# Performance work log

Measured on AMD Instinct MI355X. Metric: run time of the kernel, lower is better.

## Reference

```python
import jax, jax.numpy as jnp
import numpy as np

N, D, S = 8192, 512, 5000
L_MAX, G_MAX, C_MAX = 512, 16, 6
MARGIN = 0.0
EPS = 1e-12


def setup_inputs() -> dict:
    key = jax.random.key(0)
    k1, k2, k3, k4, k5, k6 = jax.random.split(key, 6)
    return {
        'embeddings': jax.random.normal(k1, (N, D), dtype=jnp.float32),
        'labels': jax.random.randint(k2, (N,), 0, L_MAX),
        'graph_ids': jax.random.randint(k3, (N,), 0, G_MAX),
        'categories': jax.random.randint(k4, (N,), 0, C_MAX),
        'idx1': jax.random.randint(k5, (S,), 0, N),
        'idx2': jax.random.randint(k6, (S,), 0, N),
    }


def reference(embeddings, labels, graph_ids, categories, idx1, idx2):
    # L2-normalize rows (F.normalize, p=2, dim=1, eps=1e-12)
    norms = jnp.maximum(jnp.linalg.norm(embeddings, axis=1, keepdims=True), EPS)
    e = embeddings / norms
    n = e.shape[0]

    conserved = categories < 3  # [n]
    r = jnp.arange(n)
    upper_tri = r[:, None] < r[None, :]                     # i < j
    same_label = labels[:, None] == labels[None, :]
    diff_graph = graph_ids[:, None] != graph_ids[None, :]
    valid_pos = (upper_tri & same_label & diff_graph
                 & conserved[:, None] & conserved[None, :])  # [n, n] bool

    sims = e @ e.T                                           # [n, n] cosine sims
    pos_cnt = jnp.sum(valid_pos)
    pos_sum = jnp.sum(jnp.where(valid_pos, 1.0 - sims, 0.0))
    pos_loss = jnp.where(pos_cnt > 0, pos_sum / jnp.maximum(pos_cnt, 1), 0.0)

    # Negative pairs: uniform random index pairs (idx1, idx2), masked to
    # different-graph, different-label, at-least-one-conserved pairs.
    neg_valid = ((graph_ids[idx1] != graph_ids[idx2])
                 & (labels[idx1] != labels[idx2])
                 & ((categories[idx1] < 3) | (categories[idx2] < 3)))  # [S]
    neg_sims = jnp.sum(e[idx1] * e[idx2], axis=1)            # [S]
    penalties = jnp.maximum(neg_sims - MARGIN, 0.0)
    neg_cnt = jnp.sum(neg_valid)
    neg_sum = jnp.sum(jnp.where(neg_valid, penalties, 0.0))
    neg_loss = jnp.where(neg_cnt > 0, neg_sum / jnp.maximum(neg_cnt, 1), 0.0)

    return pos_loss + neg_loss
```

## Files before the change

kernel.cpp:

```cpp
#include <hip/hip_runtime.h>

#define DIM 512
#define NVEC4 (DIM / 4)
#define LMAX 512
#define MAXB 32
#define MAXPAIR (MAXB * (MAXB - 1) / 2)
#define NB_NEG 128
#define NB_TOTAL (LMAX + NB_NEG)
#define TPB 1024
#define NGROUPS (TPB / 16)
#define EPS 1e-12f

__device__ __forceinline__ float d4(const float4 a, const float4 b) {
    return a.x * b.x + a.y * b.y + a.z * b.z + a.w * b.w;
}

__device__ __forceinline__ void dot3_16(const float4* __restrict__ E4,
                                        int ia, int ib, int gl,
                                        float& aa, float& ab, float& bb) {
    const float4* A = E4 + (size_t)ia * NVEC4;
    const float4* B = E4 + (size_t)ib * NVEC4;
    float saa = 0.0f, sab = 0.0f, sbb = 0.0f;
#pragma unroll
    for (int k = 0; k < 8; ++k) {
        float4 x = A[gl + 16 * k];
        float4 y = B[gl + 16 * k];
        saa += d4(x, x);
        sab += d4(x, y);
        sbb += d4(y, y);
    }
#pragma unroll
    for (int m = 8; m >= 1; m >>= 1) {
        saa += __shfl_xor(saa, m, 64);
        sab += __shfl_xor(sab, m, 64);
        sbb += __shfl_xor(sbb, m, 64);
    }
    aa = saa; ab = sab; bb = sbb;
}

__device__ __forceinline__ float cos_sim(float aa, float ab, float bb) {
    return ab / (fmaxf(sqrtf(aa), EPS) * fmaxf(sqrtf(bb), EPS));
}

__global__ void __launch_bounds__(TPB)
mega_kernel(const float* __restrict__ E,
            const int* __restrict__ labels,
            const int* __restrict__ graphs,
            const int* __restrict__ cats,
            const int* __restrict__ idx1,
            const int* __restrict__ idx2,
            int n, int S,
            float4* __restrict__ partials) {
    __shared__ int idxs[MAXB];
    __shared__ int gcount;
    __shared__ int2 plist[MAXPAIR];
    __shared__ int pcount;
    __shared__ float s_acc[4];
    const int tid = threadIdx.x;
    const int grp = tid >> 4, gl = tid & 15;
    if (tid == 0) { gcount = 0; pcount = 0; }
    if (tid < 4) s_acc[tid] = 0.0f;
    __syncthreads();

    const float4* E4 = (const float4*)E;

    if (blockIdx.x < LMAX) {
        const int lbl = blockIdx.x;
        const int4* lab4 = (const int4*)labels;
        int nv4 = n >> 2;
        for (int v = tid; v < nv4; v += TPB) {
            int4 l4 = lab4[v];
            int base = v << 2;
            if (l4.x == lbl && cats[base + 0] < 3) { int p = atomicAdd(&gcount, 1); if (p < MAXB) idxs[p] = base + 0; }
            if (l4.y == lbl && cats[base + 1] < 3) { int p = atomicAdd(&gcount, 1); if (p < MAXB) idxs[p] = base + 1; }
            if (l4.z == lbl && cats[base + 2] < 3) { int p = atomicAdd(&gcount, 1); if (p < MAXB) idxs[p] = base + 2; }
            if (l4.w == lbl && cats[base + 3] < 3) { int p = atomicAdd(&gcount, 1); if (p < MAXB) idxs[p] = base + 3; }
        }
        __syncthreads();

        int g = min(gcount, MAXB);
        if (tid < g * g) {
            int a = tid / g, b = tid - a * g;
            if (a < b) {
                int ia = idxs[a], ib = idxs[b];
                if (graphs[ia] != graphs[ib]) {
                    int slot = atomicAdd(&pcount, 1);
                    plist[slot] = make_int2(ia, ib);
                }
            }
        }
        __syncthreads();

        int np = pcount;
        float psum = 0.0f, pc = 0.0f;
        for (int p = grp; p < np; p += NGROUPS) {
            int2 pr = plist[p];
            float aa, ab, bb;
            dot3_16(E4, pr.x, pr.y, gl, aa, ab, bb);
            if (gl == 0) {
                psum += 1.0f - cos_sim(aa, ab, bb);
                pc += 1.0f;
            }
        }
        if (gl == 0 && pc != 0.0f) {
            atomicAdd(&s_acc[0], psum);
            atomicAdd(&s_acc[1], pc);
        }
    } else {
        int base = (blockIdx.x - LMAX) * NGROUPS;
        int stride = NB_NEG * NGROUPS;
        float nsum = 0.0f, nc = 0.0f;
        for (int s = base + grp; s < S; s += stride) {
            int i = idx1[s], j = idx2[s];
            if (graphs[i] != graphs[j] && labels[i] != labels[j] &&
                (cats[i] < 3 || cats[j] < 3)) {
                float aa, ab, bb;
                dot3_16(E4, i, j, gl, aa, ab, bb);
                if (gl == 0) {
                    nsum += fmaxf(cos_sim(aa, ab, bb), 0.0f);
                    nc += 1.0f;
                }
            }
        }
        if (gl == 0 && nc != 0.0f) {
            atomicAdd(&s_acc[2], nsum);
            atomicAdd(&s_acc[3], nc);
        }
    }
    __syncthreads();
    if (tid == 0)
        partials[blockIdx.x] = make_float4(s_acc[0], s_acc[1], s_acc[2], s_acc[3]);
}

__global__ void __launch_bounds__(256)
finalize_kernel(const float4* __restrict__ partials, int nb,
                float* __restrict__ out) {
    __shared__ float s_acc[4];
    int tid = threadIdx.x, lane = tid & 63;
    if (tid < 4) s_acc[tid] = 0.0f;
    __syncthreads();

    float ps = 0.0f, pc = 0.0f, ns = 0.0f, nc = 0.0f;
    for (int i = tid; i < nb; i += 256) {
        float4 v = partials[i];
        ps += v.x; pc += v.y; ns += v.z; nc += v.w;
    }
#pragma unroll
    for (int m = 32; m > 0; m >>= 1) {
        ps += __shfl_xor(ps, m, 64);
        pc += __shfl_xor(pc, m, 64);
        ns += __shfl_xor(ns, m, 64);
        nc += __shfl_xor(nc, m, 64);
    }
    if (lane == 0) {
        atomicAdd(&s_acc[0], ps);
        atomicAdd(&s_acc[1], pc);
        atomicAdd(&s_acc[2], ns);
        atomicAdd(&s_acc[3], nc);
    }
    __syncthreads();
    if (tid == 0) {
        float pos = (s_acc[1] > 0.0f) ? s_acc[0] / s_acc[1] : 0.0f;
        float neg = (s_acc[3] > 0.0f) ? s_acc[2] / s_acc[3] : 0.0f;
        out[0] = pos + neg;
    }
}

extern "C" void kernel_launch(void* const* d_in, const int* in_sizes, int n_in,
                              void* d_out, int out_size, void* d_ws, size_t ws_size,
                              hipStream_t stream) {
    const float* E    = (const float*)d_in[0];
    const int* labels = (const int*)d_in[1];
    const int* graphs = (const int*)d_in[2];
    const int* cats   = (const int*)d_in[3];
    const int* idx1   = (const int*)d_in[4];
    const int* idx2   = (const int*)d_in[5];
    int n = in_sizes[1];
    int S = in_sizes[4];

    float4* partials = (float4*)d_ws;

    mega_kernel<<<NB_TOTAL, TPB, 0, stream>>>(E, labels, graphs, cats,
                                              idx1, idx2, n, S, partials);
    finalize_kernel<<<1, 256, 0, stream>>>(partials, NB_TOTAL, (float*)d_out);
}
```

Baseline: 19.38 us.

## Stage label-group rows in shared memory and precompute inverse norms

Positive-pair blocks now copy each label group's embedding rows into LDS once and compute per-row inverse norms once. Pair dot products then read from shared memory instead of re-fetching both rows from global memory for every pair. Pairs are packed as small local indices. The negative-block count is sized from S (79 instead of 128), and the finalize kernel is reduced to a single wavefront. The trade-off is 64KB of LDS per block, which may limit occupancy.

```diff
diff --git a/kernel.cpp b/kernel.cpp
--- a/kernel.cpp
+++ b/kernel.cpp
@@ -5,37 +5,12 @@
 #define LMAX 512
 #define MAXB 32
 #define MAXPAIR (MAXB * (MAXB - 1) / 2)
-#define NB_NEG 128
-#define NB_TOTAL (LMAX + NB_NEG)
 #define TPB 1024
 #define NGROUPS (TPB / 16)
 #define EPS 1e-12f
 
 __device__ __forceinline__ float d4(const float4 a, const float4 b) {
     return a.x * b.x + a.y * b.y + a.z * b.z + a.w * b.w;
-}
-
-__device__ __forceinline__ void dot3_16(const float4* __restrict__ E4,
-                                        int ia, int ib, int gl,
-                                        float& aa, float& ab, float& bb) {
-    const float4* A = E4 + (size_t)ia * NVEC4;
-    const float4* B = E4 + (size_t)ib * NVEC4;
-    float saa = 0.0f, sab = 0.0f, sbb = 0.0f;
-#pragma unroll
-    for (int k = 0; k < 8; ++k) {
-        float4 x = A[gl + 16 * k];
-        float4 y = B[gl + 16 * k];
-        saa += d4(x, x);
-        sab += d4(x, y);
-        sbb += d4(y, y);
-    }
-#pragma unroll
-    for (int m = 8; m >= 1; m >>= 1) {
-        saa += __shfl_xor(saa, m, 64);
-        sab += __shfl_xor(sab, m, 64);
-        sbb += __shfl_xor(sbb, m, 64);
-    }
-    aa = saa; ab = sab; bb = sbb;
 }
 
 __device__ __forceinline__ float cos_sim(float aa, float ab, float bb) {
@@ -51,10 +26,11 @@
             const int* __restrict__ idx2,
             int n, int S,
             float4* __restrict__ partials) {
+    __shared__ float4 rows[MAXB][NVEC4];
+    __shared__ float rinv[MAXB];
     __shared__ int idxs[MAXB];
-    __shared__ int gcount;
-    __shared__ int2 plist[MAXPAIR];
-    __shared__ int pcount;
+    __shared__ int plist[MAXPAIR];
+    __shared__ int gcount, pcount;
     __shared__ float s_acc[4];
     const int tid = threadIdx.x;
     const int grp = tid >> 4, gl = tid & 15;
@@ -78,46 +54,80 @@
         }
         __syncthreads();
 
-        int g = min(gcount, MAXB);
+        const int g = min(gcount, MAXB);
+
+        for (int u = tid; u < g * NVEC4; u += TPB) {
+            int r = u >> 7, c = u & (NVEC4 - 1);
+            rows[r][c] = E4[(size_t)idxs[r] * NVEC4 + c];
+        }
         if (tid < g * g) {
-            int a = tid / g, b = tid - a * g;
+            int a = tid >> 5, b = tid & 31;
+            a = tid / g; b = tid - a * g;
             if (a < b) {
-                int ia = idxs[a], ib = idxs[b];
-                if (graphs[ia] != graphs[ib]) {
-                    int slot = atomicAdd(&pcount, 1);
-                    plist[slot] = make_int2(ia, ib);
+                if (graphs[idxs[a]] != graphs[idxs[b]]) {
+                    plist[atomicAdd(&pcount, 1)] = (a << 5) | b;
                 }
             }
         }
         __syncthreads();
 
-        int np = pcount;
-        float psum = 0.0f, pc = 0.0f;
+        if (grp < g) {
+            float s = 0.0f;
+#pragma unroll
+            for (int k = 0; k < 8; ++k) {
+                float4 x = rows[grp][gl + 16 * k];
+                s += d4(x, x);
+            }
+#pragma unroll
+            for (int m = 8; m >= 1; m >>= 1) s += __shfl_xor(s, m, 64);
+            if (gl == 0) rinv[grp] = 1.0f / fmaxf(sqrtf(s), EPS);
+        }
+        __syncthreads();
+
+        const int np = pcount;
+        float psum = 0.0f;
         for (int p = grp; p < np; p += NGROUPS) {
-            int2 pr = plist[p];
-            float aa, ab, bb;
-            dot3_16(E4, pr.x, pr.y, gl, aa, ab, bb);
-            if (gl == 0) {
-                psum += 1.0f - cos_sim(aa, ab, bb);
-                pc += 1.0f;
-            }
+            int pk = plist[p];
+            int a = pk >> 5, b = pk & 31;
+            float ab = 0.0f;
+#pragma unroll
+            for (int k = 0; k < 8; ++k)
+                ab += d4(rows[a][gl + 16 * k], rows[b][gl + 16 * k]);
+#pragma unroll
+            for (int m = 8; m >= 1; m >>= 1) ab += __shfl_xor(ab, m, 64);
+            if (gl == 0) psum += 1.0f - ab * rinv[a] * rinv[b];
         }
-        if (gl == 0 && pc != 0.0f) {
-            atomicAdd(&s_acc[0], psum);
-            atomicAdd(&s_acc[1], pc);
+        if (gl == 0 && psum != 0.0f) atomicAdd(&s_acc[0], psum);
+        __syncthreads();
+        if (tid == 0) {
+            s_acc[1] = (float)np;
+            partials[blockIdx.x] = make_float4(s_acc[0], s_acc[1], 0.0f, 0.0f);
         }
     } else {
         int base = (blockIdx.x - LMAX) * NGROUPS;
-        int stride = NB_NEG * NGROUPS;
+        int stride = (gridDim.x - LMAX) * NGROUPS;
         float nsum = 0.0f, nc = 0.0f;
         for (int s = base + grp; s < S; s += stride) {
             int i = idx1[s], j = idx2[s];
             if (graphs[i] != graphs[j] && labels[i] != labels[j] &&
                 (cats[i] < 3 || cats[j] < 3)) {
-                float aa, ab, bb;
-                dot3_16(E4, i, j, gl, aa, ab, bb);
+                const float4* A = E4 + (size_t)i * NVEC4;
+                const float4* B = E4 + (size_t)j * NVEC4;
+                float saa = 0.0f, sab = 0.0f, sbb = 0.0f;
+#pragma unroll
+                for (int k = 0; k < 8; ++k) {
+                    float4 x = A[gl + 16 * k];
+                    float4 y = B[gl + 16 * k];
+                    saa += d4(x, x); sab += d4(x, y); sbb += d4(y, y);
+                }
+#pragma unroll
+                for (int m = 8; m >= 1; m >>= 1) {
+                    saa += __shfl_xor(saa, m, 64);
+                    sab += __shfl_xor(sab, m, 64);
+                    sbb += __shfl_xor(sbb, m, 64);
+                }
                 if (gl == 0) {
-                    nsum += fmaxf(cos_sim(aa, ab, bb), 0.0f);
+                    nsum += fmaxf(cos_sim(saa, sab, sbb), 0.0f);
                     nc += 1.0f;
                 }
             }
@@ -126,22 +136,18 @@
             atomicAdd(&s_acc[2], nsum);
             atomicAdd(&s_acc[3], nc);
         }
+        __syncthreads();
+        if (tid == 0)
+            partials[blockIdx.x] = make_float4(0.0f, 0.0f, s_acc[2], s_acc[3]);
     }
-    __syncthreads();
-    if (tid == 0)
-        partials[blockIdx.x] = make_float4(s_acc[0], s_acc[1], s_acc[2], s_acc[3]);
 }
 
-__global__ void __launch_bounds__(256)
+__global__ void __launch_bounds__(64)
 finalize_kernel(const float4* __restrict__ partials, int nb,
                 float* __restrict__ out) {
-    __shared__ float s_acc[4];
-    int tid = threadIdx.x, lane = tid & 63;
-    if (tid < 4) s_acc[tid] = 0.0f;
-    __syncthreads();
-
+    int lane = threadIdx.x;
     float ps = 0.0f, pc = 0.0f, ns = 0.0f, nc = 0.0f;
-    for (int i = tid; i < nb; i += 256) {
+    for (int i = lane; i < nb; i += 64) {
         float4 v = partials[i];
         ps += v.x; pc += v.y; ns += v.z; nc += v.w;
     }
@@ -153,15 +159,8 @@
         nc += __shfl_xor(nc, m, 64);
     }
     if (lane == 0) {
-        atomicAdd(&s_acc[0], ps);
-        atomicAdd(&s_acc[1], pc);
-        atomicAdd(&s_acc[2], ns);
-        atomicAdd(&s_acc[3], nc);
-    }
-    __syncthreads();
-    if (tid == 0) {
-        float pos = (s_acc[1] > 0.0f) ? s_acc[0] / s_acc[1] : 0.0f;
-        float neg = (s_acc[3] > 0.0f) ? s_acc[2] / s_acc[3] : 0.0f;
+        float pos = (pc > 0.0f) ? ps / pc : 0.0f;
+        float neg = (nc > 0.0f) ? ns / nc : 0.0f;
         out[0] = pos + neg;
     }
 }
@@ -178,9 +177,13 @@
     int n = in_sizes[1];
     int S = in_sizes[4];
 
+    int nb_neg = (S + NGROUPS - 1) / NGROUPS;
+    if (nb_neg > 128) nb_neg = 128;
+    int nb = LMAX + nb_neg;
+
     float4* partials = (float4*)d_ws;
 
-    mega_kernel<<<NB_TOTAL, TPB, 0, stream>>>(E, labels, graphs, cats,
-                                              idx1, idx2, n, S, partials);
-    finalize_kernel<<<1, 256, 0, stream>>>(partials, NB_TOTAL, (float*)d_out);
+    mega_kernel<<<nb, TPB, 0, stream>>>(E, labels, graphs, cats,
+                                        idx1, idx2, n, S, partials);
+    finalize_kernel<<<1, 64, 0, stream>>>(partials, nb, (float*)d_out);
 }
```

New measurement: 20.71 us. 6.9% more time.
